# Optimization experiments

Measured on AMD Instinct MI355X. Metric: run time of the kernel, lower is better.

The kernel has to match this reference:

```python
import jax, jax.numpy as jnp
import numpy as np

N_NODES = 50000
N_EDGES = 600000
D = 128
DROP_P = 0.5


def setup_inputs() -> dict:
    key = jax.random.key(0)
    k1, k2, k3, k4, k5, k6 = jax.random.split(key, 6)
    x = jax.random.normal(k1, (N_NODES, D), dtype=jnp.float32)
    W = jax.random.normal(k2, (D, D), dtype=jnp.float32) * (1.0 / np.sqrt(D))
    b = jax.random.normal(k3, (D,), dtype=jnp.float32) * 0.01
    mask_u = jax.random.uniform(k4, (N_NODES, D), dtype=jnp.float32)
    src = jax.random.randint(k5, (N_EDGES,), 0, N_NODES, dtype=jnp.int64)
    dst = jax.random.randint(k6, (N_EDGES,), 0, N_NODES, dtype=jnp.int64)
    return {"x": x, "W": W, "b": b, "mask_u": mask_u, "src": src, "dst": dst}


def reference(x, W, b, mask_u, src, dst):
    n_nodes = x.shape[0]
    # linear + relu (nn.Linear stores weight as [out, in]; here W is [out, in])
    h = jax.nn.relu(jnp.einsum('nd,od->no', x, W) + b)
    # inverted dropout with precomputed uniform noise (train mode, p=0.5)
    keep = (mask_u >= DROP_P).astype(h.dtype)
    h = h * keep * (1.0 / (1.0 - DROP_P))
    # message passing: msg = h[src], reduce = sum over incoming edges per dst
    msgs = jnp.take(h, src, axis=0)            # [E, D] gather
    out = jax.ops.segment_sum(msgs, dst, num_segments=n_nodes)  # [N, D]
    return out
```

## Files before the change

### kernel.cpp

```cpp
#include <hip/hip_runtime.h>

#define D 128
#define TILE_N 16
#define HPITCH 132
#define RNODES 256
#define FCAP 48
#define LCAP 32
#define SPILL_MAX 8192

typedef __attribute__((ext_vector_type(8))) short  short8;
typedef __attribute__((ext_vector_type(4))) float  f32x4;

__device__ inline unsigned short f32_to_bf16(float f) {
    unsigned int u = __float_as_uint(f);
    unsigned int r = (u + 0x7FFFu + ((u >> 16) & 1u)) >> 16;
    return (unsigned short)r;
}
__device__ inline float bf16_to_f32(unsigned short s) {
    return __uint_as_float(((unsigned int)s) << 16);
}
__device__ inline short8 pack_bf16x8(float4 a, float4 b) {
    short8 u;
    u[0] = (short)f32_to_bf16(a.x); u[1] = (short)f32_to_bf16(a.y);
    u[2] = (short)f32_to_bf16(a.z); u[3] = (short)f32_to_bf16(a.w);
    u[4] = (short)f32_to_bf16(b.x); u[5] = (short)f32_to_bf16(b.y);
    u[6] = (short)f32_to_bf16(b.z); u[7] = (short)f32_to_bf16(b.w);
    return u;
}

__global__ __launch_bounds__(256) void prep_kernel(
    const float* __restrict__ W, unsigned short* __restrict__ Wb,
    const float* __restrict__ x, unsigned short* __restrict__ xb,
    const float* __restrict__ mask_u, unsigned char* __restrict__ mbits,
    int n_nodes, int* __restrict__ spill_cnt)
{
    const int tid = blockIdx.x * 256 + threadIdx.x;
    const int nth = gridDim.x * 256;

    for (int i = tid; i < (D * D) / 8; i += nth) {
        float4 v0 = *(const float4*)&W[i * 8];
        float4 v1 = *(const float4*)&W[i * 8 + 4];
        *(short8*)&Wb[i * 8] = pack_bf16x8(v0, v1);
    }
    const int nx8 = n_nodes * (D / 8);
    for (int i = tid; i < nx8; i += nth) {
        float4 v0 = *(const float4*)&x[(size_t)i * 8];
        float4 v1 = *(const float4*)&x[(size_t)i * 8 + 4];
        *(short8*)&xb[(size_t)i * 8] = pack_bf16x8(v0, v1);
    }
    for (int i = tid; i < nx8; i += nth) {
        float4 m0 = *(const float4*)&mask_u[(size_t)i * 8];
        float4 m1 = *(const float4*)&mask_u[(size_t)i * 8 + 4];
        unsigned b = 0;
        b |= (m0.x >= 0.5f) ? 1u : 0u;   b |= (m0.y >= 0.5f) ? 2u : 0u;
        b |= (m0.z >= 0.5f) ? 4u : 0u;   b |= (m0.w >= 0.5f) ? 8u : 0u;
        b |= (m1.x >= 0.5f) ? 16u : 0u;  b |= (m1.y >= 0.5f) ? 32u : 0u;
        b |= (m1.z >= 0.5f) ? 64u : 0u;  b |= (m1.w >= 0.5f) ? 128u : 0u;
        mbits[i] = (unsigned char)b;
    }
    if (tid == 0) *spill_cnt = 0;
}

__global__ __launch_bounds__(256) void binpass1_kernel(
    const int* __restrict__ src, const int* __restrict__ dst,
    int n_edges, int chunk, int n_ranges,
    unsigned int* __restrict__ seg, int* __restrict__ cnt_grid,
    int* __restrict__ spill_cnt, int* __restrict__ spill)
{
    __shared__ int s_fcnt[RNODES];
    __shared__ unsigned int s_fifo[RNODES * FCAP];
    const int b = blockIdx.x;
    const int t = threadIdx.x;
    const int nb = gridDim.x;

    for (int i = t; i < n_ranges; i += 256) s_fcnt[i] = 0;
    __syncthreads();

    const int e0 = b * chunk;
    const int e1 = (e0 + chunk < n_edges) ? e0 + chunk : n_edges;
    for (int i = e0 + t; i < e1; i += 256) {
        int dd = dst[i];
        int ss = src[i];
        int r  = dd >> 8;
        int pos = atomicAdd(&s_fcnt[r], 1);
        if (pos < FCAP) {
            s_fifo[r * FCAP + pos] = ((unsigned)dd << 16) | (unsigned)ss;
        } else {
            int k = atomicAdd(spill_cnt, 1);
            if (k < SPILL_MAX) { spill[2 * k] = dd; spill[2 * k + 1] = ss; }
        }
    }
    __syncthreads();

    for (int f = t; f < n_ranges * FCAP; f += 256) {
        int r = f / FCAP, slot = f - r * FCAP;
        if (slot < s_fcnt[r])
            seg[((size_t)r * nb + b) * FCAP + slot] = s_fifo[f];
    }
    for (int r = t; r < n_ranges; r += 256) {
        int c = s_fcnt[r];
        cnt_grid[r * nb + b] = (c > FCAP) ? FCAP : c;
    }
}

__global__ __launch_bounds__(256, 8) void mega_kernel(
    const unsigned short* __restrict__ xb, const unsigned short* __restrict__ Wb,
    const float* __restrict__ bias, const unsigned char* __restrict__ mbits,
    unsigned short* __restrict__ h, int n_nodes,
    const unsigned int* __restrict__ seg, const int* __restrict__ cnt_grid,
    int nb1, int n_ranges,
    int* __restrict__ deg, unsigned short* __restrict__ bucket,
    int* __restrict__ spill_cnt, int* __restrict__ spill)
{
    __shared__ __align__(16) char smem[19712];
    const int t = threadIdx.x;

    if ((int)blockIdx.x < n_ranges) {
        int* s_pref = (int*)smem;
        int* s_cnt  = (int*)(smem + 1024);
        int* s_ncnt = (int*)(smem + 2048);
        unsigned short* s_slots = (unsigned short*)(smem + 3072);
        const int r = blockIdx.x;
        const unsigned rbase = (unsigned)r << 8;

        int v = (t < nb1) ? cnt_grid[r * nb1 + t] : 0;
        s_pref[t] = v;
        s_cnt[t]  = v;
        s_ncnt[t] = 0;
        __syncthreads();
        for (int o = 1; o < 256; o <<= 1) {
            int add = (t >= o) ? s_pref[t - o] : 0;
            __syncthreads();
            s_pref[t] += add;
            __syncthreads();
        }
        const int total = s_pref[255];

        for (int f = t; f < total; f += 256) {
            int lo = 0, hi = nb1 - 1;
            while (lo < hi) {
                int mid = (lo + hi) >> 1;
                if (s_pref[mid] > f) hi = mid; else lo = mid + 1;
            }
            int slot = f - (s_pref[lo] - s_cnt[lo]);
            unsigned pk = seg[((size_t)r * nb1 + lo) * FCAP + slot];
            unsigned dd = pk >> 16;
            unsigned ss = pk & 0xFFFFu;
            int rel = (int)(dd - rbase);
            int pos = atomicAdd(&s_ncnt[rel], 1);
            if (pos < LCAP) {
                s_slots[(rel << 5) + pos] = (unsigned short)ss;
            } else {
                int k = atomicAdd(spill_cnt, 1);
                if (k < SPILL_MAX) { spill[2 * k] = (int)dd; spill[2 * k + 1] = (int)ss; }
            }
        }
        __syncthreads();

        const int node = (int)rbase + t;
        if (node < n_nodes) {
            int c = s_ncnt[t];
            deg[node] = (c > LCAP) ? LCAP : c;
        }
        for (int vv = t; vv < 1024; vv += 256) {
            int rel = vv >> 2;
            int gn  = (int)rbase + rel;
            if (gn < n_nodes)
                *(short8*)&bucket[((size_t)gn << 5) + ((vv & 3) << 3)] =
                    *(const short8*)&s_slots[vv << 3];
        }
    } else {
        unsigned short* ht = (unsigned short*)smem;
        const int lane = t & 63;
        const int w    = t >> 6;
        const int fr   = lane & 15;
        const int fg   = lane >> 4;
        const int n0 = (blockIdx.x - n_ranges) * TILE_N;

        const int prow = t >> 4;
        const int pcg  = t & 15;
        const int pnode = n0 + prow;
        const bool pvalid = (pnode < n_nodes);
        unsigned mbyte = 0;
        if (pvalid) mbyte = mbits[pnode * 16 + pcg];

        int arow = n0 + fr;
        if (arow >= n_nodes) arow = n_nodes - 1;
        const unsigned short* xr = xb + (size_t)arow * D;
        short8 a0 = *(const short8*)&xr[ 0 + fg * 8];
        short8 a1 = *(const short8*)&xr[32 + fg * 8];
        short8 a2 = *(const short8*)&xr[64 + fg * 8];
        short8 a3 = *(const short8*)&xr[96 + fg * 8];

        const float bs0 = bias[32 * w + fr];
        const float bs1 = bias[32 * w + 16 + fr];
        const unsigned short* wb0 = Wb + (size_t)(32 * w + fr) * D;
        const unsigned short* wb1 = Wb + (size_t)(32 * w + 16 + fr) * D;

        f32x4 acc0 = (f32x4){0.f, 0.f, 0.f, 0.f};
        f32x4 acc1 = (f32x4){0.f, 0.f, 0.f, 0.f};
        #pragma unroll
        for (int s = 0; s < 4; ++s) {
            short8 a = (s == 0) ? a0 : (s == 1) ? a1 : (s == 2) ? a2 : a3;
            short8 b0 = *(const short8*)&wb0[s * 32 + fg * 8];
            short8 b1 = *(const short8*)&wb1[s * 32 + fg * 8];
            acc0 = __builtin_amdgcn_mfma_f32_16x16x32_bf16(a, b0, acc0, 0, 0, 0);
            acc1 = __builtin_amdgcn_mfma_f32_16x16x32_bf16(a, b1, acc1, 0, 0, 0);
        }

        #pragma unroll
        for (int rr = 0; rr < 4; ++rr) {
            const int rl = fg * 4 + rr;
            float v0 = fmaxf(acc0[rr] + bs0, 0.f);
            float v1 = fmaxf(acc1[rr] + bs1, 0.f);
            ht[rl * HPITCH + 32 * w + fr]      = f32_to_bf16(v0);
            ht[rl * HPITCH + 32 * w + 16 + fr] = f32_to_bf16(v1);
        }
        __syncthreads();

        if (pvalid) {
            short8 hv = *(const short8*)&ht[prow * HPITCH + pcg * 8];
            short8 o;
            #pragma unroll
            for (int j = 0; j < 8; ++j) {
                float v = bf16_to_f32((unsigned short)hv[j]) * 2.f;
                o[j] = ((mbyte >> j) & 1u) ? (short)f32_to_bf16(v) : (short)0;
            }
            *(short8*)&h[(size_t)pnode * D + pcg * 8] = o;
        }
    }
}

__global__ __launch_bounds__(256) void gather_reduce_kernel(
    const unsigned short* __restrict__ h, const int* __restrict__ deg,
    const unsigned short* __restrict__ bucket, float* __restrict__ out,
    int n_nodes)
{
    const int t = threadIdx.x;
    const int node = blockIdx.x * 16 + (t >> 4);
    if (node >= n_nodes) return;
    const int cb = (t & 15) * 8;
    int dg = deg[node];
    if (dg > LCAP) dg = LCAP;
    const unsigned short* b = bucket + ((size_t)node << 5);

    float acc[8];
    #pragma unroll
    for (int j = 0; j < 8; ++j) acc[j] = 0.f;

    int i = 0;
    for (; i + 3 < dg; i += 4) {
        int s0 = b[i], s1 = b[i + 1], s2 = b[i + 2], s3 = b[i + 3];
        short8 v0 = *(const short8*)&h[(size_t)s0 * D + cb];
        short8 v1 = *(const short8*)&h[(size_t)s1 * D + cb];
        short8 v2 = *(const short8*)&h[(size_t)s2 * D + cb];
        short8 v3 = *(const short8*)&h[(size_t)s3 * D + cb];
        #pragma unroll
        for (int j = 0; j < 8; ++j)
            acc[j] += (bf16_to_f32((unsigned short)v0[j]) +
                       bf16_to_f32((unsigned short)v1[j])) +
                      (bf16_to_f32((unsigned short)v2[j]) +
                       bf16_to_f32((unsigned short)v3[j]));
    }
    for (; i < dg; ++i) {
        int s0 = b[i];
        short8 v0 = *(const short8*)&h[(size_t)s0 * D + cb];
        #pragma unroll
        for (int j = 0; j < 8; ++j) acc[j] += bf16_to_f32((unsigned short)v0[j]);
    }

    f32x4 o0 = (f32x4){acc[0], acc[1], acc[2], acc[3]};
    f32x4 o1 = (f32x4){acc[4], acc[5], acc[6], acc[7]};
    __builtin_nontemporal_store(o0, (f32x4*)&out[(size_t)node * D + cb]);
    __builtin_nontemporal_store(o1, (f32x4*)&out[(size_t)node * D + cb + 4]);
}

__global__ __launch_bounds__(256) void spill_apply_kernel(
    const unsigned short* __restrict__ h, const int* __restrict__ spill_cnt,
    const int* __restrict__ spill, float* __restrict__ out)
{
    int n = *spill_cnt;
    if (n > SPILL_MAX) n = SPILL_MAX;
    for (int e = (int)(threadIdx.x >> 4); e < n; e += 16) {
        int dd = spill[2 * e], ss = spill[2 * e + 1];
        int cb = (threadIdx.x & 15) * 8;
        short8 v = *(const short8*)&h[(size_t)ss * D + cb];
        float* o = &out[(size_t)dd * D + cb];
        #pragma unroll
        for (int j = 0; j < 8; ++j)
            atomicAdd(o + j, bf16_to_f32((unsigned short)v[j]));
    }
}

__global__ __launch_bounds__(256) void zero_kernel(int* __restrict__ p, int n)
{
    int i = blockIdx.x * 256 + threadIdx.x;
    if (i < n) p[i] = 0;
}

__global__ __launch_bounds__(256) void gemm_fb_kernel(
    const float* __restrict__ x, const float* __restrict__ W,
    const float* __restrict__ bias, const float* __restrict__ mask_u,
    unsigned short* __restrict__ h, int n_nodes)
{
    int tid = blockIdx.x * 256 + threadIdx.x;
    if (tid >= n_nodes * 16) return;
    int node = tid >> 4, cg = tid & 15;
    for (int c = 0; c < 8; ++c) {
        int col = cg * 8 + c;
        float s = bias[col];
        for (int k = 0; k < D; ++k)
            s += bf16_to_f32(f32_to_bf16(x[(size_t)node * D + k])) *
                 bf16_to_f32(f32_to_bf16(W[(size_t)col * D + k]));
        s = fmaxf(s, 0.f);
        float m = mask_u[(size_t)node * D + col];
        s *= (m >= 0.5f) ? 2.f : 0.f;
        h[(size_t)node * D + col] = f32_to_bf16(s);
    }
}

__global__ __launch_bounds__(256) void scatter_atomic_kernel(
    const unsigned short* __restrict__ h, const int* __restrict__ src,
    const int* __restrict__ dst, float* __restrict__ out, int n_edges)
{
    const int t = threadIdx.x;
    const int e = blockIdx.x * 16 + (t >> 4);
    if (e >= n_edges) return;
    const int cb = (t & 15) * 8;
    const int s  = src[e];
    const int dd = dst[e];
    short8 v = *(const short8*)&h[(size_t)s * D + cb];
    float* o = &out[(size_t)dd * D + cb];
    #pragma unroll
    for (int j = 0; j < 8; ++j) atomicAdd(o + j, bf16_to_f32((unsigned short)v[j]));
}

extern "C" void kernel_launch(void* const* d_in, const int* in_sizes, int n_in,
                              void* d_out, int out_size, void* d_ws, size_t ws_size,
                              hipStream_t stream) {
    const float* x      = (const float*)d_in[0];
    const float* W      = (const float*)d_in[1];
    const float* bias   = (const float*)d_in[2];
    const float* mask_u = (const float*)d_in[3];
    const int*   src    = (const int*)d_in[4];
    const int*   dst    = (const int*)d_in[5];
    float* out = (float*)d_out;

    const int n_nodes  = in_sizes[0] / D;
    const int n_edges  = in_sizes[4];
    const int n_tiles  = (n_nodes + TILE_N - 1) / TILE_N;
    const int n_ranges = (n_nodes + RNODES - 1) / RNODES;
    const int nb1      = n_ranges;
    const int chunk    = (n_edges + nb1 - 1) / nb1;

    const size_t wb_bytes = (size_t)D * D * sizeof(unsigned short);
    const size_t xb_bytes = (size_t)n_nodes * D * sizeof(unsigned short);
    const size_t h_bytes  = (size_t)n_nodes * D * sizeof(unsigned short);
    char* p = (char*)d_ws;
    unsigned short* Wb = (unsigned short*)p;     p += wb_bytes;
    unsigned short* xb = (unsigned short*)p;     p += xb_bytes;
    unsigned short* h  = (unsigned short*)p;     p += h_bytes;
    int* deg       = (int*)p;                    p += (size_t)((n_nodes + 3) & ~3) * sizeof(int);
    int* spill_cnt = (int*)p;                    p += 16;
    int* spill     = (int*)p;                    p += (size_t)2 * SPILL_MAX * sizeof(int);
    unsigned short* bucket = (unsigned short*)p; p += (size_t)n_nodes * LCAP * sizeof(unsigned short);
    unsigned int* seg      = (unsigned int*)p;   p += (size_t)n_ranges * nb1 * FCAP * sizeof(unsigned int);
    int* cnt_grid  = (int*)p;                    p += (size_t)n_ranges * nb1 * sizeof(int);
    unsigned char* mbits = (unsigned char*)p;    p += (size_t)n_nodes * 16;
    const size_t needed = (size_t)(p - (char*)d_ws);

    if (ws_size >= needed && n_nodes <= 65535) {
        prep_kernel<<<2048, 256, 0, stream>>>(
            W, Wb, x, xb, mask_u, mbits, n_nodes, spill_cnt);
        binpass1_kernel<<<nb1, 256, 0, stream>>>(
            src, dst, n_edges, chunk, n_ranges, seg, cnt_grid, spill_cnt, spill);
        mega_kernel<<<n_ranges + n_tiles, 256, 0, stream>>>(
            xb, Wb, bias, mbits, h, n_nodes,
            seg, cnt_grid, nb1, n_ranges, deg, bucket, spill_cnt, spill);
        gather_reduce_kernel<<<(n_nodes + 15) / 16, 256, 0, stream>>>(
            h, deg, bucket, out, n_nodes);
        spill_apply_kernel<<<1, 256, 0, stream>>>(h, spill_cnt, spill, out);
    } else {
        unsigned short* hf = (unsigned short*)d_ws;
        gemm_fb_kernel<<<(n_nodes * 16 + 255) / 256, 256, 0, stream>>>(
            x, W, bias, mask_u, hf, n_nodes);
        zero_kernel<<<(out_size + 255) / 256, 256, 0, stream>>>((int*)d_out, out_size);
        scatter_atomic_kernel<<<(n_edges + 15) / 16, 256, 0, stream>>>(
            hf, src, dst, out, n_edges);
    }
}
```

Baseline: 77.29 us.

## Fuse prep and edge binning into one launch, convert x to bf16 inline

Merges the weight/mask conversion kernel and the first edge-binning pass into a single launch, with separate block ranges doing each job so the two run concurrently. The x-to-bf16 conversion pass is removed, and the GEMM tiles now read fp32 x directly and pack to bf16 in registers. This saves a full write and read of a bf16 copy of x and one kernel launch. In exchange it adds a tiny zero kernel for the spill counter, and the GEMM reads twice as many bytes of x.

```diff
diff --git a/kernel.cpp b/kernel.cpp
--- a/kernel.cpp
+++ b/kernel.cpp
@@ -28,83 +28,85 @@
     return u;
 }
 
-__global__ __launch_bounds__(256) void prep_kernel(
+__global__ __launch_bounds__(256) void zero_kernel(int* __restrict__ p, int n)
+{
+    int i = blockIdx.x * 256 + threadIdx.x;
+    if (i < n) p[i] = 0;
+}
+
+__global__ __launch_bounds__(256) void prepbin_kernel(
     const float* __restrict__ W, unsigned short* __restrict__ Wb,
-    const float* __restrict__ x, unsigned short* __restrict__ xb,
     const float* __restrict__ mask_u, unsigned char* __restrict__ mbits,
-    int n_nodes, int* __restrict__ spill_cnt)
-{
-    const int tid = blockIdx.x * 256 + threadIdx.x;
-    const int nth = gridDim.x * 256;
-
-    for (int i = tid; i < (D * D) / 8; i += nth) {
-        float4 v0 = *(const float4*)&W[i * 8];
-        float4 v1 = *(const float4*)&W[i * 8 + 4];
-        *(short8*)&Wb[i * 8] = pack_bf16x8(v0, v1);
-    }
-    const int nx8 = n_nodes * (D / 8);
-    for (int i = tid; i < nx8; i += nth) {
-        float4 v0 = *(const float4*)&x[(size_t)i * 8];
-        float4 v1 = *(const float4*)&x[(size_t)i * 8 + 4];
-        *(short8*)&xb[(size_t)i * 8] = pack_bf16x8(v0, v1);
-    }
-    for (int i = tid; i < nx8; i += nth) {
-        float4 m0 = *(const float4*)&mask_u[(size_t)i * 8];
-        float4 m1 = *(const float4*)&mask_u[(size_t)i * 8 + 4];
-        unsigned b = 0;
-        b |= (m0.x >= 0.5f) ? 1u : 0u;   b |= (m0.y >= 0.5f) ? 2u : 0u;
-        b |= (m0.z >= 0.5f) ? 4u : 0u;   b |= (m0.w >= 0.5f) ? 8u : 0u;
-        b |= (m1.x >= 0.5f) ? 16u : 0u;  b |= (m1.y >= 0.5f) ? 32u : 0u;
-        b |= (m1.z >= 0.5f) ? 64u : 0u;  b |= (m1.w >= 0.5f) ? 128u : 0u;
-        mbits[i] = (unsigned char)b;
-    }
-    if (tid == 0) *spill_cnt = 0;
-}
-
-__global__ __launch_bounds__(256) void binpass1_kernel(
+    int n_nodes,
     const int* __restrict__ src, const int* __restrict__ dst,
     int n_edges, int chunk, int n_ranges,
     unsigned int* __restrict__ seg, int* __restrict__ cnt_grid,
     int* __restrict__ spill_cnt, int* __restrict__ spill)
 {
-    __shared__ int s_fcnt[RNODES];
-    __shared__ unsigned int s_fifo[RNODES * FCAP];
-    const int b = blockIdx.x;
+    __shared__ __align__(16) char smem[50176];
     const int t = threadIdx.x;
-    const int nb = gridDim.x;
-
-    for (int i = t; i < n_ranges; i += 256) s_fcnt[i] = 0;
-    __syncthreads();
-
-    const int e0 = b * chunk;
-    const int e1 = (e0 + chunk < n_edges) ? e0 + chunk : n_edges;
-    for (int i = e0 + t; i < e1; i += 256) {
-        int dd = dst[i];
-        int ss = src[i];
-        int r  = dd >> 8;
-        int pos = atomicAdd(&s_fcnt[r], 1);
-        if (pos < FCAP) {
-            s_fifo[r * FCAP + pos] = ((unsigned)dd << 16) | (unsigned)ss;
-        } else {
-            int k = atomicAdd(spill_cnt, 1);
-            if (k < SPILL_MAX) { spill[2 * k] = dd; spill[2 * k + 1] = ss; }
-        }
-    }
-    __syncthreads();
-
-    for (int f = t; f < n_ranges * FCAP; f += 256) {
-        int r = f / FCAP, slot = f - r * FCAP;
-        if (slot < s_fcnt[r])
-            seg[((size_t)r * nb + b) * FCAP + slot] = s_fifo[f];
-    }
-    for (int r = t; r < n_ranges; r += 256) {
-        int c = s_fcnt[r];
-        cnt_grid[r * nb + b] = (c > FCAP) ? FCAP : c;
+
+    if ((int)blockIdx.x < n_ranges) {
+        int* s_fcnt = (int*)smem;
+        unsigned int* s_fifo = (unsigned int*)(smem + 1024);
+        const int b  = blockIdx.x;
+        const int nb = n_ranges;
+
+        for (int i = t; i < n_ranges; i += 256) s_fcnt[i] = 0;
+        __syncthreads();
+
+        const int e0 = b * chunk;
+        const int e1 = (e0 + chunk < n_edges) ? e0 + chunk : n_edges;
+        for (int i = e0 + t; i < e1; i += 256) {
+            int dd = dst[i];
+            int ss = src[i];
+            int r  = dd >> 8;
+            int pos = atomicAdd(&s_fcnt[r], 1);
+            if (pos < FCAP) {
+                s_fifo[r * FCAP + pos] = ((unsigned)dd << 16) | (unsigned)ss;
+            } else {
+                int k = atomicAdd(spill_cnt, 1);
+                if (k < SPILL_MAX) { spill[2 * k] = dd; spill[2 * k + 1] = ss; }
+            }
+        }
+        __syncthreads();
+
+        for (int f = t; f < n_ranges * FCAP; f += 256) {
+            int r = f / FCAP, slot = f - r * FCAP;
+            if (slot < s_fcnt[r])
+                seg[((size_t)r * nb + b) * FCAP + slot] = s_fifo[f];
+        }
+        for (int r = t; r < n_ranges; r += 256) {
+            int c = s_fcnt[r];
+            cnt_grid[r * nb + b] = (c > FCAP) ? FCAP : c;
+        }
+    } else {
+        const int bid = blockIdx.x - n_ranges;
+        const int nconv = gridDim.x - n_ranges;
+        const int tid = bid * 256 + t;
+        const int nth = nconv * 256;
+
+        for (int i = tid; i < (D * D) / 8; i += nth) {
+            float4 v0 = *(const float4*)&W[i * 8];
+            float4 v1 = *(const float4*)&W[i * 8 + 4];
+            *(short8*)&Wb[i * 8] = pack_bf16x8(v0, v1);
+        }
+        const int nx8 = n_nodes * (D / 8);
+        for (int i = tid; i < nx8; i += nth) {
+            float4 m0 = *(const float4*)&mask_u[(size_t)i * 8];
+            float4 m1 = *(const float4*)&mask_u[(size_t)i * 8 + 4];
+            unsigned b = 0;
+            b |= (m0.x >= 0.5f) ? 1u : 0u;   b |= (m0.y >= 0.5f) ? 2u : 0u;
+            b |= (m0.z >= 0.5f) ? 4u : 0u;   b |= (m0.w >= 0.5f) ? 8u : 0u;
+            b |= (m1.x >= 0.5f) ? 16u : 0u;  b |= (m1.y >= 0.5f) ? 32u : 0u;
+            b |= (m1.z >= 0.5f) ? 64u : 0u;  b |= (m1.w >= 0.5f) ? 128u : 0u;
+            mbits[i] = (unsigned char)b;
+        }
     }
 }
 
 __global__ __launch_bounds__(256, 8) void mega_kernel(
-    const unsigned short* __restrict__ xb, const unsigned short* __restrict__ Wb,
+    const float* __restrict__ x, const unsigned short* __restrict__ Wb,
     const float* __restrict__ bias, const unsigned char* __restrict__ mbits,
     unsigned short* __restrict__ h, int n_nodes,
     const unsigned int* __restrict__ seg, const int* __restrict__ cnt_grid,
@@ -186,11 +188,15 @@
 
         int arow = n0 + fr;
         if (arow >= n_nodes) arow = n_nodes - 1;
-        const unsigned short* xr = xb + (size_t)arow * D;
-        short8 a0 = *(const short8*)&xr[ 0 + fg * 8];
-        short8 a1 = *(const short8*)&xr[32 + fg * 8];
-        short8 a2 = *(const short8*)&xr[64 + fg * 8];
-        short8 a3 = *(const short8*)&xr[96 + fg * 8];
+        const float* xr = x + (size_t)arow * D;
+        short8 a0 = pack_bf16x8(*(const float4*)&xr[ 0 + fg * 8],
+                                *(const float4*)&xr[ 4 + fg * 8]);
+        short8 a1 = pack_bf16x8(*(const float4*)&xr[32 + fg * 8],
+                                *(const float4*)&xr[36 + fg * 8]);
+        short8 a2 = pack_bf16x8(*(const float4*)&xr[64 + fg * 8],
+                                *(const float4*)&xr[68 + fg * 8]);
+        short8 a3 = pack_bf16x8(*(const float4*)&xr[96 + fg * 8],
+                                *(const float4*)&xr[100 + fg * 8]);
 
         const float bs0 = bias[32 * w + fr];
         const float bs1 = bias[32 * w + 16 + fr];
@@ -290,12 +296,6 @@
         for (int j = 0; j < 8; ++j)
             atomicAdd(o + j, bf16_to_f32((unsigned short)v[j]));
     }
-}
-
-__global__ __launch_bounds__(256) void zero_kernel(int* __restrict__ p, int n)
-{
-    int i = blockIdx.x * 256 + threadIdx.x;
-    if (i < n) p[i] = 0;
 }
 
 __global__ __launch_bounds__(256) void gemm_fb_kernel(
@@ -354,11 +354,9 @@
     const int chunk    = (n_edges + nb1 - 1) / nb1;
 
     const size_t wb_bytes = (size_t)D * D * sizeof(unsigned short);
-    const size_t xb_bytes = (size_t)n_nodes * D * sizeof(unsigned short);
     const size_t h_bytes  = (size_t)n_nodes * D * sizeof(unsigned short);
     char* p = (char*)d_ws;
     unsigned short* Wb = (unsigned short*)p;     p += wb_bytes;
-    unsigned short* xb = (unsigned short*)p;     p += xb_bytes;
     unsigned short* h  = (unsigned short*)p;     p += h_bytes;
     int* deg       = (int*)p;                    p += (size_t)((n_nodes + 3) & ~3) * sizeof(int);
     int* spill_cnt = (int*)p;                    p += 16;
@@ -370,12 +368,12 @@
     const size_t needed = (size_t)(p - (char*)d_ws);
 
     if (ws_size >= needed && n_nodes <= 65535) {
-        prep_kernel<<<2048, 256, 0, stream>>>(
-            W, Wb, x, xb, mask_u, mbits, n_nodes, spill_cnt);
-        binpass1_kernel<<<nb1, 256, 0, stream>>>(
+        zero_kernel<<<1, 256, 0, stream>>>(spill_cnt, 4);
+        prepbin_kernel<<<n_ranges + 1024, 256, 0, stream>>>(
+            W, Wb, mask_u, mbits, n_nodes,
             src, dst, n_edges, chunk, n_ranges, seg, cnt_grid, spill_cnt, spill);
         mega_kernel<<<n_ranges + n_tiles, 256, 0, stream>>>(
-            xb, Wb, bias, mbits, h, n_nodes,
+            x, Wb, bias, mbits, h, n_nodes,
             seg, cnt_grid, nb1, n_ranges, deg, bucket, spill_cnt, spill);
         gather_reduce_kernel<<<(n_nodes + 15) / 16, 256, 0, stream>>>(
             h, deg, bucket, out, n_nodes);
```

New measurement: 76.59 us. No clear change (-0.9%).
